# Optimization experiments

Measured on AMD Instinct MI355X. Metric: run time of the kernel, lower is better.

Reference implementation:

```python
import jax, jax.numpy as jnp
import numpy as np

VOCAB = 29
VEC = 512      # vector_dim
HID = 1024     # hidden_size
SEN = 64       # sen_len (== seq length)
BATCH = 2048


def setup_inputs() -> dict:
    key = jax.random.key(0)
    k1, k2, k3, k4, k5, k6 = jax.random.split(key, 6)
    s_emb = 1.0
    s_ih = 1.0 / np.sqrt(HID)
    s_cls = 1.0 / np.sqrt(HID)
    return {
        "x": jax.random.randint(k1, (BATCH, SEN), 0, VOCAB, dtype=jnp.int64),
        "emb": jax.random.normal(k2, (VOCAB, VEC), dtype=jnp.float32) * s_emb,
        "W_ih": jax.random.uniform(k3, (HID, VEC), dtype=jnp.float32, minval=-s_ih, maxval=s_ih),
        "W_hh": jax.random.uniform(k4, (HID, HID), dtype=jnp.float32, minval=-s_ih, maxval=s_ih),
        "W_cls": jax.random.uniform(k5, (SEN + 1, HID), dtype=jnp.float32, minval=-s_cls, maxval=s_cls),
        "b_cls": jax.random.uniform(k6, (SEN + 1,), dtype=jnp.float32, minval=-s_cls, maxval=s_cls),
    }


def reference(x, emb, W_ih, W_hh, W_cls, b_cls):
    # Embedding lookup: [B, S, VEC]
    xe = emb[x]
    # Precompute input projections for all timesteps: [B, S, HID]
    xin = jnp.einsum("bsv,hv->bsh", xe, W_ih)

    def step(h, x_t):
        # h: [B, HID], x_t: [B, HID] (already W_ih @ x)
        h_new = jnp.tanh(x_t + h @ W_hh.T)
        return h_new, None

    h0 = jnp.zeros((x.shape[0], HID), dtype=xin.dtype)
    h_last, _ = jax.lax.scan(step, h0, jnp.swapaxes(xin, 0, 1))  # scan over S

    # h.squeeze() in torch (num_layers=1) -> [B, HID]
    logits = h_last @ W_cls.T + b_cls  # [B, SEN+1]
    return logits
```

## Files before the change

### kernel.cpp

```cpp
#include <hip/hip_runtime.h>
#include <hip/hip_bf16.h>

#define VOCAB 29
#define VEC   512
#define HID   1024
#define SEN   64
#define BATCH 2048

typedef __bf16 bf16_t;
typedef bf16_t bf16x8 __attribute__((ext_vector_type(8)));
typedef float  floatx4 __attribute__((ext_vector_type(4)));

__global__ void cvt_whh(const float* __restrict__ w, bf16_t* __restrict__ o, int n) {
    int i = blockIdx.x * blockDim.x + threadIdx.x;
    if (i < n) o[i] = (bf16_t)w[i];
}

__global__ void cvt_wcls(const float* __restrict__ w, bf16_t* __restrict__ o) {
    int i = blockIdx.x * blockDim.x + threadIdx.x;
    if (i >= 80 * HID) return;
    o[i] = (i < 65 * HID) ? (bf16_t)w[i] : (bf16_t)0.0f;
}

__global__ void proj_kernel(const float* __restrict__ emb, const float* __restrict__ wih,
                            float* __restrict__ proj) {
    int idx = blockIdx.x * blockDim.x + threadIdx.x;
    if (idx >= VOCAB * HID) return;
    int v = idx / HID, h = idx % HID;
    const float* e = emb + v * VEC;
    const float* w = wih + h * VEC;
    float s = 0.f;
    for (int k = 0; k < VEC; k += 4) {
        float4 ev = *(const float4*)(e + k);
        float4 wv = *(const float4*)(w + k);
        s += ev.x * wv.x + ev.y * wv.y + ev.z * wv.z + ev.w * wv.w;
    }
    proj[idx] = s;
}

__device__ __forceinline__ float fast_tanh(float x) {
    float e = __expf(2.0f * x);
    return 1.0f - 2.0f / (e + 1.0f);
}

__device__ __forceinline__ void load16_to_lds(const bf16_t* g, bf16_t* l) {
    auto gp = reinterpret_cast<const __attribute__((address_space(1))) unsigned int*>(
        reinterpret_cast<uintptr_t>(g));
    auto lp = reinterpret_cast<__attribute__((address_space(3))) unsigned int*>(
        static_cast<unsigned int>(reinterpret_cast<uintptr_t>(l)));
    __builtin_amdgcn_global_load_lds(gp, lp, 16, 0, 0);
}

#define BM 128
#define BN 64
#define BK 64

__global__ __launch_bounds__(256)
void rnn_step(const bf16_t* __restrict__ h_in, const bf16_t* __restrict__ whh,
              const float* __restrict__ proj, const int* __restrict__ x,
              bf16_t* __restrict__ h_out, int t, int first)
{
    __shared__ __align__(16) bf16_t Ash[2][BM][BK];
    __shared__ __align__(16) bf16_t Bsh[2][BN][BK];
    __shared__ int tok_sh[BM];

    const int tid  = threadIdx.x;
    const int m0   = blockIdx.x * BM;
    const int n0   = blockIdx.y * BN;
    const int wave = tid >> 6;
    const int lane = tid & 63;
    const int wm   = wave * 32;
    const int q    = lane >> 4;
    const int l16  = lane & 15;

    if (tid < BM) tok_sh[tid] = x[(m0 + tid) * SEN + t];

    const bf16_t* srcA[4];
    const bf16_t* srcB[2];
    int dstA[4], dstB[2];
#pragma unroll
    for (int it = 0; it < 4; it++) {
        int c = it * 256 + wave * 64 + lane;
        int r = c >> 3, p = c & 7, g = p ^ (r & 7);
        srcA[it] = h_in + (m0 + r) * HID + g * 8;
        dstA[it] = (it * 256 + wave * 64) * 8;
    }
#pragma unroll
    for (int it = 0; it < 2; it++) {
        int c = it * 256 + wave * 64 + lane;
        int r = c >> 3, p = c & 7, g = p ^ (r & 7);
        srcB[it] = whh + (n0 + r) * HID + g * 8;
        dstB[it] = (it * 256 + wave * 64) * 8;
    }

    floatx4 acc[2][4];
#pragma unroll
    for (int i = 0; i < 2; i++)
#pragma unroll
        for (int j = 0; j < 4; j++) acc[i][j] = (floatx4){0.f, 0.f, 0.f, 0.f};

    if (!first) {
#pragma unroll
        for (int it = 0; it < 4; it++) load16_to_lds(srcA[it], &Ash[0][0][0] + dstA[it]);
#pragma unroll
        for (int it = 0; it < 2; it++) load16_to_lds(srcB[it], &Bsh[0][0][0] + dstB[it]);
    }
    __syncthreads();

    if (!first) {
        for (int i = 0; i < 16; i++) {
            const int buf = i & 1;
            if (i < 15) {
                const int koff = (i + 1) * BK;
#pragma unroll
                for (int it = 0; it < 4; it++)
                    load16_to_lds(srcA[it] + koff, &Ash[1 - buf][0][0] + dstA[it]);
#pragma unroll
                for (int it = 0; it < 2; it++)
                    load16_to_lds(srcB[it] + koff, &Bsh[1 - buf][0][0] + dstB[it]);
            }
#pragma unroll
            for (int ks = 0; ks < BK; ks += 32) {
                const int pq = (((ks >> 3) + q) ^ (l16 & 7)) * 8;
                bf16x8 af[2], bfr[4];
                af[0]  = *(const bf16x8*)&Ash[buf][wm + l16][pq];
                af[1]  = *(const bf16x8*)&Ash[buf][wm + 16 + l16][pq];
                bfr[0] = *(const bf16x8*)&Bsh[buf][l16][pq];
                bfr[1] = *(const bf16x8*)&Bsh[buf][16 + l16][pq];
                bfr[2] = *(const bf16x8*)&Bsh[buf][32 + l16][pq];
                bfr[3] = *(const bf16x8*)&Bsh[buf][48 + l16][pq];
#pragma unroll
                for (int mi = 0; mi < 2; mi++)
#pragma unroll
                    for (int ni = 0; ni < 4; ni++)
                        acc[mi][ni] = __builtin_amdgcn_mfma_f32_16x16x32_bf16(
                            af[mi], bfr[ni], acc[mi][ni], 0, 0, 0);
            }
            if (i < 15) __syncthreads();
        }
    }

#pragma unroll
    for (int mi = 0; mi < 2; mi++) {
#pragma unroll
        for (int r = 0; r < 4; r++) {
            int lm = wm + mi * 16 + q * 4 + r;
            int gm = m0 + lm;
            const float* pr = proj + tok_sh[lm] * HID;
#pragma unroll
            for (int ni = 0; ni < 4; ni++) {
                int gn = n0 + ni * 16 + l16;
                float v = acc[mi][ni][r] + pr[gn];
                h_out[gm * HID + gn] = (bf16_t)fast_tanh(v);
            }
        }
    }
}

#define CBM 128
#define CLDK 72
__global__ __launch_bounds__(256)
void classifier_mfma(const bf16_t* __restrict__ h, const bf16_t* __restrict__ wcls,
                     const float* __restrict__ bcls, float* __restrict__ out)
{
    __shared__ __align__(16) bf16_t Ash[CBM][CLDK];
    __shared__ __align__(16) bf16_t Bsh[80][CLDK];

    const int tid = threadIdx.x;
    const int m0 = blockIdx.x * CBM;
    const int wave = tid >> 6, lane = tid & 63;
    const int wm = wave * 32;
    const int q = lane >> 4, l16 = lane & 15;

    floatx4 acc[2][5];
#pragma unroll
    for (int i = 0; i < 2; i++)
#pragma unroll
        for (int j = 0; j < 5; j++) acc[i][j] = (floatx4){0.f, 0.f, 0.f, 0.f};

    for (int kk = 0; kk < HID; kk += 64) {
#pragma unroll
        for (int it = 0; it < 4; it++) {
            int idx = tid + it * 256, r = idx >> 3, c = (idx & 7) * 8;
            *(uint4*)&Ash[r][c] = *(const uint4*)&h[(m0 + r) * HID + kk + c];
        }
#pragma unroll
        for (int it = 0; it < 3; it++) {
            int idx = tid + it * 256;
            if (idx < 640) {
                int r = idx >> 3, c = (idx & 7) * 8;
                *(uint4*)&Bsh[r][c] = *(const uint4*)&wcls[r * HID + kk + c];
            }
        }
        __syncthreads();
#pragma unroll
        for (int ks = 0; ks < 64; ks += 32) {
            bf16x8 af[2], bfr[5];
#pragma unroll
            for (int mi = 0; mi < 2; mi++)
                af[mi] = *(const bf16x8*)&Ash[wm + mi * 16 + l16][ks + q * 8];
#pragma unroll
            for (int ni = 0; ni < 5; ni++)
                bfr[ni] = *(const bf16x8*)&Bsh[ni * 16 + l16][ks + q * 8];
#pragma unroll
            for (int mi = 0; mi < 2; mi++)
#pragma unroll
                for (int ni = 0; ni < 5; ni++)
                    acc[mi][ni] = __builtin_amdgcn_mfma_f32_16x16x32_bf16(
                        af[mi], bfr[ni], acc[mi][ni], 0, 0, 0);
        }
        __syncthreads();
    }

#pragma unroll
    for (int mi = 0; mi < 2; mi++) {
#pragma unroll
        for (int r = 0; r < 4; r++) {
            int gm = m0 + wm + mi * 16 + q * 4 + r;
#pragma unroll
            for (int ni = 0; ni < 5; ni++) {
                int gn = ni * 16 + l16;
                if (gn < SEN + 1)
                    out[gm * (SEN + 1) + gn] = acc[mi][ni][r] + bcls[gn];
            }
        }
    }
}

extern "C" void kernel_launch(void* const* d_in, const int* in_sizes, int n_in,
                              void* d_out, int out_size, void* d_ws, size_t ws_size,
                              hipStream_t stream)
{
    const int*   x     = (const int*)  d_in[0];
    const float* emb   = (const float*)d_in[1];
    const float* w_ih  = (const float*)d_in[2];
    const float* w_hh  = (const float*)d_in[3];
    const float* w_cls = (const float*)d_in[4];
    const float* b_cls = (const float*)d_in[5];
    float* out = (float*)d_out;

    char* ws = (char*)d_ws;
    bf16_t* whh_bf  = (bf16_t*)ws;
    float*  proj    = (float*)(ws + (2u << 20));
    bf16_t* wcls_bf = (bf16_t*)(ws + (2u << 20) + (128u << 10));
    bf16_t* h0      = (bf16_t*)(ws + (2u << 20) + (288u << 10));
    bf16_t* h1      = (bf16_t*)(ws + (6u << 20) + (288u << 10));

    cvt_whh<<<(HID * HID) / 256, 256, 0, stream>>>(w_hh, whh_bf, HID * HID);
    proj_kernel<<<(VOCAB * HID + 255) / 256, 256, 0, stream>>>(emb, w_ih, proj);
    cvt_wcls<<<(80 * HID) / 256, 256, 0, stream>>>(w_cls, wcls_bf);

    dim3 grid(BATCH / BM, HID / BN);
    bf16_t* bufs[2] = {h0, h1};
    for (int t = 0; t < SEN; t++) {
        bf16_t* hi = bufs[(t + 1) & 1];
        bf16_t* ho = bufs[t & 1];
        rnn_step<<<grid, 256, 0, stream>>>(hi, whh_bf, proj, x, ho, t, t == 0 ? 1 : 0);
    }
    classifier_mfma<<<BATCH / CBM, 256, 0, stream>>>(bufs[1], wcls_bf, b_cls, out);
}
```

Measured before the change: 782.6 us.

## Replace per-timestep launches with persistent cooperative RNN kernel and per-row-block flags

```diff
diff --git a/kernel.cpp b/kernel.cpp
--- a/kernel.cpp
+++ b/kernel.cpp
@@ -43,12 +43,134 @@
     return 1.0f - 2.0f / (e + 1.0f);
 }
 
-__device__ __forceinline__ void load16_to_lds(const bf16_t* g, bf16_t* l) {
+__device__ __forceinline__ void load16_to_lds(const bf16_t* g, bf16_t* l, int aux) {
     auto gp = reinterpret_cast<const __attribute__((address_space(1))) unsigned int*>(
         reinterpret_cast<uintptr_t>(g));
     auto lp = reinterpret_cast<__attribute__((address_space(3))) unsigned int*>(
         static_cast<unsigned int>(reinterpret_cast<uintptr_t>(l)));
-    __builtin_amdgcn_global_load_lds(gp, lp, 16, 0, 0);
+    if (aux) __builtin_amdgcn_global_load_lds(gp, lp, 16, 0, 1);
+    else     __builtin_amdgcn_global_load_lds(gp, lp, 16, 0, 0);
+}
+
+#define PBM 128
+#define PBN 64
+#define PBK 32
+#define BSTRIDE 1032
+
+__global__ __launch_bounds__(256, 1)
+void rnn_persist(const bf16_t* __restrict__ whh_bf, const float* __restrict__ proj,
+                 const int* __restrict__ x, bf16_t* __restrict__ h0b,
+                 bf16_t* __restrict__ h1b, int* __restrict__ flags)
+{
+    extern __shared__ __align__(16) char smem[];
+    bf16_t* Bs  = (bf16_t*)smem;
+    bf16_t* As  = (bf16_t*)(smem + 132096);
+    float*  psh = (float*) (smem + 132096 + 16384);
+    int*    tsh = (int*)   (smem + 132096 + 16384 + 7424);
+
+    const int tid  = threadIdx.x;
+    const int bx   = blockIdx.x, by = blockIdx.y;
+    const int m0   = bx * PBM, n0 = by * PBN;
+    const int wave = tid >> 6, lane = tid & 63;
+    const int wm   = wave * 32;
+    const int q    = lane >> 4, l16 = lane & 15;
+
+#pragma unroll 4
+    for (int it = 0; it < 32; it++) {
+        int c0 = it * 256 + wave * 64;
+        int c  = c0 + lane;
+        int r  = c >> 7, cc = c & 127;
+        load16_to_lds(whh_bf + (n0 + r) * HID + cc * 8,
+                      Bs + (c0 >> 7) * BSTRIDE + (c0 & 127) * 8, 0);
+    }
+    for (int i = tid; i < VOCAB * 64; i += 256) {
+        int v = i >> 6, j = i & 63;
+        psh[v * 64 + j] = proj[v * HID + n0 + j];
+    }
+
+    int baseA[2], dstA[2];
+#pragma unroll
+    for (int it = 0; it < 2; it++) {
+        int c = it * 256 + wave * 64 + lane;
+        int r = c >> 2, p = c & 3, g = p ^ (r & 3);
+        baseA[it] = (m0 + r) * HID + g * 8;
+        dstA[it]  = (it * 256 + wave * 64) * 8;
+    }
+    __syncthreads();
+
+    for (int t = 0; t < SEN; t++) {
+        const bf16_t* __restrict__ hin  = (t & 1) ? h0b : h1b;
+        bf16_t* __restrict__       hout = (t & 1) ? h1b : h0b;
+
+        if (t > 0 && tid == 0) {
+            const int need = 16 * t;
+            while (__hip_atomic_load(flags + bx, __ATOMIC_RELAXED,
+                                     __HIP_MEMORY_SCOPE_AGENT) < need)
+                __builtin_amdgcn_s_sleep(4);
+        }
+        __syncthreads();
+        if (tid < PBM) tsh[tid] = x[(m0 + tid) * SEN + t];
+
+        floatx4 acc[2][4];
+#pragma unroll
+        for (int i = 0; i < 2; i++)
+#pragma unroll
+            for (int j = 0; j < 4; j++) acc[i][j] = (floatx4){0.f, 0.f, 0.f, 0.f};
+
+        if (t > 0) {
+#pragma unroll
+            for (int it = 0; it < 2; it++)
+                load16_to_lds(hin + baseA[it], As + dstA[it], 1);
+            __syncthreads();
+            for (int i = 0; i < 32; i++) {
+                const int buf = i & 1;
+                if (i < 31) {
+#pragma unroll
+                    for (int it = 0; it < 2; it++)
+                        load16_to_lds(hin + baseA[it] + (i + 1) * PBK,
+                                      As + (1 - buf) * 4096 + dstA[it], 1);
+                }
+                const int pq = (q ^ (l16 & 3)) * 8;
+                const int kb = i * PBK + q * 8;
+                bf16x8 af0 = *(const bf16x8*)(As + buf * 4096 + (wm + l16) * PBK + pq);
+                bf16x8 af1 = *(const bf16x8*)(As + buf * 4096 + (wm + 16 + l16) * PBK + pq);
+                bf16x8 b0  = *(const bf16x8*)(Bs + (     l16) * BSTRIDE + kb);
+                bf16x8 b1  = *(const bf16x8*)(Bs + (16 + l16) * BSTRIDE + kb);
+                bf16x8 b2  = *(const bf16x8*)(Bs + (32 + l16) * BSTRIDE + kb);
+                bf16x8 b3  = *(const bf16x8*)(Bs + (48 + l16) * BSTRIDE + kb);
+                acc[0][0] = __builtin_amdgcn_mfma_f32_16x16x32_bf16(af0, b0, acc[0][0], 0,0,0);
+                acc[0][1] = __builtin_amdgcn_mfma_f32_16x16x32_bf16(af0, b1, acc[0][1], 0,0,0);
+                acc[0][2] = __builtin_amdgcn_mfma_f32_16x16x32_bf16(af0, b2, acc[0][2], 0,0,0);
+                acc[0][3] = __builtin_amdgcn_mfma_f32_16x16x32_bf16(af0, b3, acc[0][3], 0,0,0);
+                acc[1][0] = __builtin_amdgcn_mfma_f32_16x16x32_bf16(af1, b0, acc[1][0], 0,0,0);
+                acc[1][1] = __builtin_amdgcn_mfma_f32_16x16x32_bf16(af1, b1, acc[1][1], 0,0,0);
+                acc[1][2] = __builtin_amdgcn_mfma_f32_16x16x32_bf16(af1, b2, acc[1][2], 0,0,0);
+                acc[1][3] = __builtin_amdgcn_mfma_f32_16x16x32_bf16(af1, b3, acc[1][3], 0,0,0);
+                __syncthreads();
+            }
+        } else {
+            __syncthreads();
+        }
+
+#pragma unroll
+        for (int mi = 0; mi < 2; mi++) {
+#pragma unroll
+            for (int r = 0; r < 4; r++) {
+                int lm = wm + mi * 16 + q * 4 + r;
+                const float* ps = psh + tsh[lm] * 64;
+                bf16_t* orow = hout + (m0 + lm) * HID + n0;
+#pragma unroll
+                for (int ni = 0; ni < 4; ni++) {
+                    float v = acc[mi][ni][r] + ps[ni * 16 + l16];
+                    orow[ni * 16 + l16] = (bf16_t)fast_tanh(v);
+                }
+            }
+        }
+        __syncthreads();
+        if (tid == 0)
+            __hip_atomic_fetch_add(flags + bx, 1, __ATOMIC_RELAXED,
+                                   __HIP_MEMORY_SCOPE_AGENT);
+    }
 }
 
 #define BM 128
@@ -101,9 +223,9 @@
 
     if (!first) {
 #pragma unroll
-        for (int it = 0; it < 4; it++) load16_to_lds(srcA[it], &Ash[0][0][0] + dstA[it]);
-#pragma unroll
-        for (int it = 0; it < 2; it++) load16_to_lds(srcB[it], &Bsh[0][0][0] + dstB[it]);
+        for (int it = 0; it < 4; it++) load16_to_lds(srcA[it], &Ash[0][0][0] + dstA[it], 0);
+#pragma unroll
+        for (int it = 0; it < 2; it++) load16_to_lds(srcB[it], &Bsh[0][0][0] + dstB[it], 0);
     }
     __syncthreads();
 
@@ -114,10 +236,10 @@
                 const int koff = (i + 1) * BK;
 #pragma unroll
                 for (int it = 0; it < 4; it++)
-                    load16_to_lds(srcA[it] + koff, &Ash[1 - buf][0][0] + dstA[it]);
+                    load16_to_lds(srcA[it] + koff, &Ash[1 - buf][0][0] + dstA[it], 0);
 #pragma unroll
                 for (int it = 0; it < 2; it++)
-                    load16_to_lds(srcB[it] + koff, &Bsh[1 - buf][0][0] + dstB[it]);
+                    load16_to_lds(srcB[it] + koff, &Bsh[1 - buf][0][0] + dstB[it], 0);
             }
 #pragma unroll
             for (int ks = 0; ks < BK; ks += 32) {
@@ -245,17 +367,33 @@
     bf16_t* wcls_bf = (bf16_t*)(ws + (2u << 20) + (128u << 10));
     bf16_t* h0      = (bf16_t*)(ws + (2u << 20) + (288u << 10));
     bf16_t* h1      = (bf16_t*)(ws + (6u << 20) + (288u << 10));
+    int*    flags   = (int*)   (ws + (10u << 20) + (288u << 10));
 
     cvt_whh<<<(HID * HID) / 256, 256, 0, stream>>>(w_hh, whh_bf, HID * HID);
     proj_kernel<<<(VOCAB * HID + 255) / 256, 256, 0, stream>>>(emb, w_ih, proj);
     cvt_wcls<<<(80 * HID) / 256, 256, 0, stream>>>(w_cls, wcls_bf);
-
-    dim3 grid(BATCH / BM, HID / BN);
-    bf16_t* bufs[2] = {h0, h1};
-    for (int t = 0; t < SEN; t++) {
-        bf16_t* hi = bufs[(t + 1) & 1];
-        bf16_t* ho = bufs[t & 1];
-        rnn_step<<<grid, 256, 0, stream>>>(hi, whh_bf, proj, x, ho, t, t == 0 ? 1 : 0);
-    }
-    classifier_mfma<<<BATCH / CBM, 256, 0, stream>>>(bufs[1], wcls_bf, b_cls, out);
-}
+    hipMemsetAsync(flags, 0, 16 * sizeof(int), stream);
+
+    const int smem_bytes = 132096 + 16384 + 7424 + 512;
+    hipError_t ce = hipFuncSetAttribute(
+        reinterpret_cast<const void*>(rnn_persist),
+        hipFuncAttributeMaxDynamicSharedMemorySize, smem_bytes);
+    if (ce == hipSuccess) {
+        void* args[] = {(void*)&whh_bf, (void*)&proj, (void*)&x,
+                        (void*)&h0, (void*)&h1, (void*)&flags};
+        ce = hipLaunchCooperativeKernel((void*)rnn_persist, dim3(16, 16),
+                                        dim3(256, 1, 1), args, smem_bytes, stream);
+    }
+    if (ce != hipSuccess) {
+        (void)hipGetLastError();
+        dim3 grid(BATCH / BM, HID / BN);
+        bf16_t* bufs[2] = {h0, h1};
+        for (int t = 0; t < SEN; t++) {
+            bf16_t* hi = bufs[(t + 1) & 1];
+            bf16_t* ho = bufs[t & 1];
+            rnn_step<<<grid, 256, 0, stream>>>(hi, whh_bf, proj, x, ho, t, t == 0 ? 1 : 0);
+        }
+    }
+
+    classifier_mfma<<<BATCH / CBM, 256, 0, stream>>>(h1, wcls_bf, b_cls, out);
+}
```

Measured after the change: 993.4 us. +26.9%, slower.
